# Kernel optimization log

Hardware: AMD Instinct MI355X
Metric: run time of the kernel (lower is better)

The kernel has to match this reference:

```python
import jax, jax.numpy as jnp
import numpy as np

IN_CH = 128
OUT_CH = 128
INPUT_LEN = 512
KERNEL = 8
STRIDE = 1
OUT_LEN = (INPUT_LEN - KERNEL) // STRIDE + 1  # 505
BATCH = 64


def setup_inputs() -> dict:
    key = jax.random.key(0)
    kx, kw, kb = jax.random.split(key, 3)
    x = jax.random.normal(kx, (BATCH, IN_CH, INPUT_LEN), dtype=jnp.float32)
    weight = jax.random.normal(kw, (OUT_LEN, OUT_CH, IN_CH, KERNEL), dtype=jnp.float32)
    bias = jax.random.normal(kb, (OUT_CH, OUT_LEN), dtype=jnp.float32)
    return {"x": x, "weight": weight, "bias": bias}


def reference(x, weight, bias):
    # unfold: gather sliding windows -> [b, i, l_out, k]
    idx = jnp.arange(OUT_LEN)[:, None] * STRIDE + jnp.arange(KERNEL)[None, :]  # [l, k]
    x_unf = x[:, :, idx]  # [b, i, l, k]
    # per-position independent GEMM: 'blik,loik->bol' with x permuted to bilk
    out = jnp.einsum('bilk,loik->bol', x_unf, weight)
    out = out + bias[None, :, :]
    return out
```

## Files before the change

### kernel.cpp

```cpp
#include <hip/hip_runtime.h>
#include <hip/hip_bf16.h>

#define BATCH 64
#define IN_CH 128
#define ILEN  512
#define OLEN  505
#define OCH   128
#define KDIM  1024
#define BK    64
#define NCHK  16
#define NWG   OLEN

typedef float f32x4  __attribute__((ext_vector_type(4)));
typedef short bf16x8 __attribute__((ext_vector_type(8)));

__device__ __forceinline__ short f2bf(float f) {
  union { __hip_bfloat16 h; short s; } u;
  u.h = __float2bfloat16(f);
  return u.s;
}

template <bool USE_TMP>
__global__ __launch_bounds__(256, 2) void lc1d_main(
    const float* __restrict__ x, const float* __restrict__ w,
    const float* __restrict__ bias, float* __restrict__ outp) {
  const int orig = blockIdx.x;
  const int xcd = orig & 7, idx = orig >> 3;
  const int q = NWG / 8, rm = NWG % 8;
  const int l = (xcd < rm ? xcd * (q + 1) : rm * (q + 1) + (xcd - rm) * q) + idx;

  const int tid  = threadIdx.x;
  const int lane = tid & 63;
  const int wn   = tid >> 6;
  const int r    = lane & 15;
  const int h    = lane >> 4;

  __shared__ float Bs[2][2][BK * 64];
  __shared__ short As[2][BK * 64];

  f32x4 acc[2][4];
#pragma unroll
  for (int oh = 0; oh < 2; ++oh)
#pragma unroll
    for (int m = 0; m < 4; ++m) acc[oh][m] = (f32x4){0.f, 0.f, 0.f, 0.f};

  const float* __restrict__ wl = w + (size_t)l * (OCH * KDIM);

  const int so  = tid >> 4;
  const int sc  = tid & 15;
  const int ssw = ((so & 7) << 1) | ((so >> 3) & 1);

  const int kk  = tid & 63;
  const int tb  = tid >> 6;
  const int il  = kk >> 3;
  const int kof = kk & 7;

  float aa0[16], aa1[16];

  auto loadA = [&](float (&aa)[16], int kc) {
    const float* xb = x + (size_t)(kc * 8 + il) * ILEN + l + kof;
#pragma unroll
    for (int it = 0; it < 16; ++it)
      aa[it] = xb[(size_t)(it * 4 + tb) * (IN_CH * ILEN)];
  };
  auto writeA = [&](const float (&aa)[16], int buf) {
#pragma unroll
    for (int it = 0; it < 16; ++it) {
      const int b = it * 4 + tb;
      As[buf][b * 64 + (kk ^ ((b & 7) << 3))] = f2bf(aa[it]);
    }
  };
  auto stageB = [&](int buf, int kc, int oh) {
    const float* wo = wl + (size_t)oh * 64 * KDIM;
#pragma unroll
    for (int it = 0; it < 4; ++it) {
      const int ob = it * 16 + so;
      const float* src = wo + (size_t)ob * KDIM + kc * BK + (sc ^ ssw) * 4;
      __builtin_amdgcn_global_load_lds(
          (const __attribute__((address_space(1))) void*)src,
          (__attribute__((address_space(3))) void*)&Bs[buf][oh][ob * 64 + sc * 4],
          16, 0, 0);
    }
  };

  const int rsw = ((r & 7) << 1) | ((r >> 3) & 1);
  auto compute = [&](int cur, int oh) {
    const int ob = wn * 16 + r;
#pragma unroll
    for (int ks = 0; ks < 2; ++ks) {
      const int c0 = ks * 8 + h * 2;
      const f32x4 blo = *reinterpret_cast<const f32x4*>(
          &Bs[cur][oh][ob * 64 + ((c0) ^ rsw) * 4]);
      const f32x4 bhi = *reinterpret_cast<const f32x4*>(
          &Bs[cur][oh][ob * 64 + ((c0 + 1) ^ rsw) * 4]);
      bf16x8 bfr;
#pragma unroll
      for (int j = 0; j < 4; ++j) {
        bfr[j]     = f2bf(blo[j]);
        bfr[4 + j] = f2bf(bhi[j]);
      }
#pragma unroll
      for (int mt = 0; mt < 4; ++mt) {
        const int b = mt * 16 + r;
        const bf16x8 afr = *reinterpret_cast<const bf16x8*>(
            &As[cur][b * 64 + ((ks * 32 + h * 8) ^ ((b & 7) << 3))]);
        acc[oh][mt] =
            __builtin_amdgcn_mfma_f32_16x16x32_bf16(afr, bfr, acc[oh][mt], 0, 0, 0);
      }
    }
  };

  loadA(aa0, 0);
  stageB(0, 0, 0);
  stageB(0, 0, 1);
  writeA(aa0, 0);
  loadA(aa1, 1);
  asm volatile("s_waitcnt vmcnt(16) lgkmcnt(0)" ::: "memory");
  __builtin_amdgcn_sched_barrier(0);
  __builtin_amdgcn_s_barrier();
  __builtin_amdgcn_sched_barrier(0);

  auto step = [&](int kc, float (&aaW)[16], float (&aaL)[16]) {
    if (kc + 1 < NCHK) {
      const int nxt = (kc + 1) & 1;
      stageB(nxt, kc + 1, 0);
      stageB(nxt, kc + 1, 1);
    }
    if (kc + 2 < NCHK) loadA(aaL, kc + 2);
    __builtin_amdgcn_sched_barrier(0);
    const int cur = kc & 1;
    compute(cur, 0);
    compute(cur, 1);
    if (kc + 1 < NCHK) {
      writeA(aaW, (kc + 1) & 1);
      if (kc + 2 < NCHK) {
        asm volatile("s_waitcnt vmcnt(16) lgkmcnt(0)" ::: "memory");
      } else {
        asm volatile("s_waitcnt vmcnt(0) lgkmcnt(0)" ::: "memory");
      }
      __builtin_amdgcn_sched_barrier(0);
      __builtin_amdgcn_s_barrier();
      __builtin_amdgcn_sched_barrier(0);
    }
  };

  for (int kc = 0; kc < NCHK; kc += 2) {
    step(kc, aa1, aa0);
    step(kc + 1, aa0, aa1);
  }

#pragma unroll
  for (int oh = 0; oh < 2; ++oh) {
    const int og = oh * 64 + wn * 16 + r;
    if (USE_TMP) {
      float* t = outp + (size_t)l * (BATCH * OCH) + og;
#pragma unroll
      for (int mt = 0; mt < 4; ++mt)
#pragma unroll
        for (int j = 0; j < 4; ++j) {
          const int b = mt * 16 + h * 4 + j;
          t[(size_t)b * OCH] = acc[oh][mt][j];
        }
    } else {
      const float bv = bias[og * OLEN + l];
#pragma unroll
      for (int mt = 0; mt < 4; ++mt)
#pragma unroll
        for (int j = 0; j < 4; ++j) {
          const int b = mt * 16 + h * 4 + j;
          outp[(size_t)b * (OCH * OLEN) + (size_t)og * OLEN + l] = acc[oh][mt][j] + bv;
        }
    }
  }
}

__global__ __launch_bounds__(256) void lc1d_tr(const float* __restrict__ tmp,
                                               const float* __restrict__ bias,
                                               float* __restrict__ out) {
  const int l0  = blockIdx.x * 64;
  const int bo0 = blockIdx.y * 64;
  const int tid = threadIdx.x;
  __shared__ float t[64][65];

  const int boj = tid & 63, lq = tid >> 6;
#pragma unroll
  for (int rr = 0; rr < 16; ++rr) {
    const int li = rr * 4 + lq;
    const int l  = l0 + li;
    if (l < OLEN) t[li][boj] = tmp[(size_t)l * (BATCH * OCH) + bo0 + boj];
  }
  __syncthreads();
  const int lj = tid & 63, bq = tid >> 6;
  const int l  = l0 + lj;
#pragma unroll
  for (int rr = 0; rr < 16; ++rr) {
    const int bl = rr * 4 + bq;
    const int bo = bo0 + bl;
    if (l < OLEN) {
      const int oc = bo & (OCH - 1);
      out[(size_t)bo * OLEN + l] = t[lj][bl] + bias[oc * OLEN + l];
    }
  }
}

extern "C" void kernel_launch(void* const* d_in, const int* in_sizes, int n_in,
                              void* d_out, int out_size, void* d_ws, size_t ws_size,
                              hipStream_t stream) {
  const float* x    = (const float*)d_in[0];
  const float* w    = (const float*)d_in[1];
  const float* bias = (const float*)d_in[2];
  float* out        = (float*)d_out;

  const size_t need = (size_t)OLEN * BATCH * OCH * sizeof(float);
  if (ws_size >= need) {
    float* tmp = (float*)d_ws;
    lc1d_main<true><<<dim3(NWG), 256, 0, stream>>>(x, w, bias, tmp);
    lc1d_tr<<<dim3(8, 128), 256, 0, stream>>>(tmp, bias, out);
  } else {
    lc1d_main<false><<<dim3(NWG), 256, 0, stream>>>(x, w, bias, out);
  }
}
```

Measured before the change: 101.7 us.

## Pre-convert input to bf16 with even/odd shifted copies for vectorized A loads

Adds a pre-pass that converts x to bf16 and stores two copies, one offset by a single element, so every sliding-window row starts 4-byte aligned. The main kernel can then load A fragments as 16-byte vectors and write them straight to LDS, instead of doing 16 scalar strided fp32 loads per thread and converting them in the loop. The A prefetch pipeline drops from two stages to one and waits on vmcnt(0) each chunk, which may expose more latency. It also costs an extra kernel launch plus the bf16 buffers, and the fallback path without enough workspace now uses a naive kernel.

```diff
diff --git a/kernel.cpp b/kernel.cpp
--- a/kernel.cpp
+++ b/kernel.cpp
@@ -11,19 +11,42 @@
 #define NCHK  16
 #define NWG   OLEN
 
-typedef float f32x4  __attribute__((ext_vector_type(4)));
-typedef short bf16x8 __attribute__((ext_vector_type(8)));
-
-__device__ __forceinline__ short f2bf(float f) {
-  union { __hip_bfloat16 h; short s; } u;
+typedef float  f32x4  __attribute__((ext_vector_type(4)));
+typedef short  bf16x8 __attribute__((ext_vector_type(8)));
+typedef unsigned short u16x8 __attribute__((ext_vector_type(8)));
+typedef u16x8 u16x8a __attribute__((aligned(4)));
+
+__device__ __forceinline__ unsigned short f2bf(float f) {
+  union { __hip_bfloat16 h; unsigned short s; } u;
   u.h = __float2bfloat16(f);
   return u.s;
 }
 
+__global__ __launch_bounds__(256) void lc1d_cvt(const float* __restrict__ x,
+                                                unsigned short* __restrict__ xbe,
+                                                unsigned short* __restrict__ xbo) {
+  const int gid = blockIdx.x * 256 + threadIdx.x;
+  const int row = gid >> 6;
+  const int t8  = (gid & 63) << 3;
+  const float* src = x + (size_t)row * ILEN + t8;
+  const f32x4 v0 = *reinterpret_cast<const f32x4*>(src);
+  const f32x4 v1 = *reinterpret_cast<const f32x4*>(src + 4);
+  const float e8 = (t8 + 8 < ILEN) ? src[8] : 0.f;
+  u16x8 e, o;
+#pragma unroll
+  for (int j = 0; j < 4; ++j) { e[j] = f2bf(v0[j]); e[4 + j] = f2bf(v1[j]); }
+  o[0] = e[1]; o[1] = e[2]; o[2] = e[3];
+  o[3] = e[4]; o[4] = e[5]; o[5] = e[6]; o[6] = e[7];
+  o[7] = f2bf(e8);
+  *reinterpret_cast<u16x8*>(xbe + (size_t)row * ILEN + t8) = e;
+  *reinterpret_cast<u16x8*>(xbo + (size_t)row * ILEN + t8) = o;
+}
+
 template <bool USE_TMP>
 __global__ __launch_bounds__(256, 2) void lc1d_main(
-    const float* __restrict__ x, const float* __restrict__ w,
-    const float* __restrict__ bias, float* __restrict__ outp) {
+    const unsigned short* __restrict__ xbe, const unsigned short* __restrict__ xbo,
+    const float* __restrict__ w, const float* __restrict__ bias,
+    float* __restrict__ outp) {
   const int orig = blockIdx.x;
   const int xcd = orig & 7, idx = orig >> 3;
   const int q = NWG / 8, rm = NWG % 8;
@@ -36,7 +59,7 @@
   const int h    = lane >> 4;
 
   __shared__ float Bs[2][2][BK * 64];
-  __shared__ short As[2][BK * 64];
+  __shared__ short As[2][BATCH * 64];
 
   f32x4 acc[2][4];
 #pragma unroll
@@ -45,30 +68,26 @@
     for (int m = 0; m < 4; ++m) acc[oh][m] = (f32x4){0.f, 0.f, 0.f, 0.f};
 
   const float* __restrict__ wl = w + (size_t)l * (OCH * KDIM);
+  const unsigned short* __restrict__ xw =
+      ((l & 1) ? xbo : xbe) + (size_t)(l & ~1);
 
   const int so  = tid >> 4;
   const int sc  = tid & 15;
   const int ssw = ((so & 7) << 1) | ((so >> 3) & 1);
-
-  const int kk  = tid & 63;
-  const int tb  = tid >> 6;
-  const int il  = kk >> 3;
-  const int kof = kk & 7;
-
-  float aa0[16], aa1[16];
-
-  auto loadA = [&](float (&aa)[16], int kc) {
-    const float* xb = x + (size_t)(kc * 8 + il) * ILEN + l + kof;
-#pragma unroll
-    for (int it = 0; it < 16; ++it)
-      aa[it] = xb[(size_t)(it * 4 + tb) * (IN_CH * ILEN)];
-  };
-  auto writeA = [&](const float (&aa)[16], int buf) {
-#pragma unroll
-    for (int it = 0; it < 16; ++it) {
-      const int b = it * 4 + tb;
-      As[buf][b * 64 + (kk ^ ((b & 7) << 3))] = f2bf(aa[it]);
-    }
+  const int bA = tid & 63;
+  const int iw = tid >> 6;
+
+  u16x8 va, vb;
+  auto loadA2 = [&](int kc) {
+    const int i0 = kc * 8 + iw * 2;
+    const unsigned short* p = xw + (size_t)(bA * IN_CH + i0) * ILEN;
+    va = *reinterpret_cast<const u16x8a*>(p);
+    vb = *reinterpret_cast<const u16x8a*>(p + ILEN);
+  };
+  auto writeA2 = [&](int buf) {
+    const int c0 = iw * 2;
+    *reinterpret_cast<u16x8*>(&As[buf][bA * 64 + ((c0 ^ (bA & 7)) << 3)]) = va;
+    *reinterpret_cast<u16x8*>(&As[buf][bA * 64 + (((c0 + 1) ^ (bA & 7)) << 3)]) = vb;
   };
   auto stageB = [&](int buf, int kc, int oh) {
     const float* wo = wl + (size_t)oh * 64 * KDIM;
@@ -96,57 +115,46 @@
       bf16x8 bfr;
 #pragma unroll
       for (int j = 0; j < 4; ++j) {
-        bfr[j]     = f2bf(blo[j]);
-        bfr[4 + j] = f2bf(bhi[j]);
+        bfr[j]     = (short)f2bf(blo[j]);
+        bfr[4 + j] = (short)f2bf(bhi[j]);
       }
 #pragma unroll
       for (int mt = 0; mt < 4; ++mt) {
         const int b = mt * 16 + r;
         const bf16x8 afr = *reinterpret_cast<const bf16x8*>(
-            &As[cur][b * 64 + ((ks * 32 + h * 8) ^ ((b & 7) << 3))]);
+            &As[cur][b * 64 + (((ks * 4 + h) ^ (r & 7)) << 3)]);
         acc[oh][mt] =
             __builtin_amdgcn_mfma_f32_16x16x32_bf16(afr, bfr, acc[oh][mt], 0, 0, 0);
       }
     }
   };
 
-  loadA(aa0, 0);
+  loadA2(0);
   stageB(0, 0, 0);
   stageB(0, 0, 1);
-  writeA(aa0, 0);
-  loadA(aa1, 1);
-  asm volatile("s_waitcnt vmcnt(16) lgkmcnt(0)" ::: "memory");
+  writeA2(0);
+  asm volatile("s_waitcnt vmcnt(0) lgkmcnt(0)" ::: "memory");
   __builtin_amdgcn_sched_barrier(0);
   __builtin_amdgcn_s_barrier();
   __builtin_amdgcn_sched_barrier(0);
 
-  auto step = [&](int kc, float (&aaW)[16], float (&aaL)[16]) {
+  for (int kc = 0; kc < NCHK; ++kc) {
+    const int cur = kc & 1, nxt = cur ^ 1;
     if (kc + 1 < NCHK) {
-      const int nxt = (kc + 1) & 1;
+      loadA2(kc + 1);
       stageB(nxt, kc + 1, 0);
       stageB(nxt, kc + 1, 1);
     }
-    if (kc + 2 < NCHK) loadA(aaL, kc + 2);
     __builtin_amdgcn_sched_barrier(0);
-    const int cur = kc & 1;
     compute(cur, 0);
     compute(cur, 1);
     if (kc + 1 < NCHK) {
-      writeA(aaW, (kc + 1) & 1);
-      if (kc + 2 < NCHK) {
-        asm volatile("s_waitcnt vmcnt(16) lgkmcnt(0)" ::: "memory");
-      } else {
-        asm volatile("s_waitcnt vmcnt(0) lgkmcnt(0)" ::: "memory");
-      }
+      writeA2(nxt);
+      asm volatile("s_waitcnt vmcnt(0) lgkmcnt(0)" ::: "memory");
       __builtin_amdgcn_sched_barrier(0);
       __builtin_amdgcn_s_barrier();
       __builtin_amdgcn_sched_barrier(0);
     }
-  };
-
-  for (int kc = 0; kc < NCHK; kc += 2) {
-    step(kc, aa1, aa0);
-    step(kc + 1, aa0, aa1);
   }
 
 #pragma unroll
@@ -203,6 +211,18 @@
   }
 }
 
+__global__ void lc1d_naive(const float* __restrict__ x, const float* __restrict__ w,
+                           const float* __restrict__ bias, float* __restrict__ out) {
+  const int l = blockIdx.x, o = blockIdx.y, b = threadIdx.x;
+  const float* wr = w + ((size_t)l * OCH + o) * KDIM;
+  const float* xr = x + (size_t)b * (IN_CH * ILEN);
+  float s = 0.f;
+  for (int i = 0; i < IN_CH; ++i)
+#pragma unroll
+    for (int k = 0; k < 8; ++k) s += xr[i * ILEN + l + k] * wr[i * 8 + k];
+  out[((size_t)b * OCH + o) * OLEN + l] = s + bias[o * OLEN + l];
+}
+
 extern "C" void kernel_launch(void* const* d_in, const int* in_sizes, int n_in,
                               void* d_out, int out_size, void* d_ws, size_t ws_size,
                               hipStream_t stream) {
@@ -211,12 +231,19 @@
   const float* bias = (const float*)d_in[2];
   float* out        = (float*)d_out;
 
-  const size_t need = (size_t)OLEN * BATCH * OCH * sizeof(float);
+  const size_t TMPB = (size_t)OLEN * BATCH * OCH * sizeof(float);
+  const size_t off1 = (TMPB + 255) & ~(size_t)255;
+  const size_t XBB  = (size_t)BATCH * IN_CH * ILEN * sizeof(short);
+  const size_t need = off1 + 2 * XBB;
+
   if (ws_size >= need) {
     float* tmp = (float*)d_ws;
-    lc1d_main<true><<<dim3(NWG), 256, 0, stream>>>(x, w, bias, tmp);
+    unsigned short* xbe = (unsigned short*)((char*)d_ws + off1);
+    unsigned short* xbo = (unsigned short*)((char*)d_ws + off1 + XBB);
+    lc1d_cvt<<<dim3(2048), 256, 0, stream>>>(x, xbe, xbo);
+    lc1d_main<true><<<dim3(NWG), 256, 0, stream>>>(xbe, xbo, w, bias, tmp);
     lc1d_tr<<<dim3(8, 128), 256, 0, stream>>>(tmp, bias, out);
   } else {
-    lc1d_main<false><<<dim3(NWG), 256, 0, stream>>>(x, w, bias, out);
-  }
-}
+    lc1d_naive<<<dim3(OLEN, OCH), BATCH, 0, stream>>>(x, w, bias, out);
+  }
+}
```

Result: slower. 105.8 us (+4.0%).
